# Kernel tuning notes

Hardware: AMD Instinct MI355X
Metric: run time of the kernel (lower is better)

The kernel has to match this reference:

```python
import jax, jax.numpy as jnp
import numpy as np

N, C, H, W = 2, 128, 64, 64
N_HEAD = 4
GROUPS = 16
EPS = 1e-5


def group_norm(x, scale, offset):
    # haiku GroupNorm, channels_first: normalize over (channels-in-group, h, w)
    n, c, h, w = x.shape
    xg = x.reshape(n, GROUPS, c // GROUPS, h, w)
    mu = xg.mean(axis=(2, 3, 4), keepdims=True)
    var = xg.var(axis=(2, 3, 4), keepdims=True)
    xg = (xg - mu) * jax.lax.rsqrt(var + EPS)
    return xg.reshape(n, c, h, w) * scale[None, :, None, None] + offset[None, :, None, None]


def setup_inputs() -> dict:
    key = jax.random.key(0)
    ks = jax.random.split(key, 4)
    inv_sqrt_c = 1.0 / np.sqrt(C).astype(np.float32)
    return {
        "x": jax.random.normal(ks[0], (N, C, H, W), dtype=jnp.float32),
        "w_qkv": jax.random.normal(ks[1], (C, 3 * C), dtype=jnp.float32) * inv_sqrt_c,
        "b_qkv": jnp.zeros((3 * C,), dtype=jnp.float32),
        "w_out": jax.random.normal(ks[2], (C, C), dtype=jnp.float32) * inv_sqrt_c,
        "b_out": jnp.zeros((C,), dtype=jnp.float32),
        "gn1_scale": jnp.ones((C,), dtype=jnp.float32),
        "gn1_offset": jnp.zeros((C,), dtype=jnp.float32),
        "gn2_scale": jnp.ones((C,), dtype=jnp.float32),
        "gn2_offset": jnp.zeros((C,), dtype=jnp.float32),
    }


def reference(x, w_qkv, b_qkv, w_out, b_out, gn1_scale, gn1_offset, gn2_scale, gn2_offset):
    n, c, h, w = x.shape
    dh = c // N_HEAD
    # GroupNorm (x is reassigned, so the residual uses the normalized x)
    xn = group_norm(x, gn1_scale, gn1_offset)
    # 1x1 conv qkv projection: [n, 3c, h, w]
    qkv = jnp.einsum('nchw,cd->ndhw', xn, w_qkv) + b_qkv[None, :, None, None]
    # [n, 3H, dh, hw] -> [n, 3H, hw, dh]
    qkv = jnp.swapaxes(qkv.reshape(n, N_HEAD * 3, dh, h * w), 2, 3)
    q, k, v = jnp.split(qkv, 3, axis=1)  # each [n, H, hw, dh]
    scale = dh ** (-0.25)
    # [n, H, hw, hw] attention matrix (the memory-bound core)
    att = jax.nn.softmax((q * scale) @ (jnp.swapaxes(k, 2, 3) * scale), axis=3)
    y = jnp.swapaxes(att @ v, 2, 3).reshape(n, c, h, w)
    # 1x1 conv out projection + GroupNorm + residual
    out = jnp.einsum('nchw,cd->ndhw', y, w_out) + b_out[None, :, None, None]
    return xn + group_norm(out, gn2_scale, gn2_offset)
```

## Files before the change

### kernel.cpp

```cpp
#include <hip/hip_runtime.h>
#include <hip/hip_bf16.h>
#include <math.h>

constexpr int cHW   = 4096;
constexpr int cC    = 128;
constexpr int cNH   = 4;
constexpr int cDH   = 32;
constexpr float cEPS = 1e-5f;
constexpr float cQS = 0.2550347805f;
constexpr int SPLIT = 4;

typedef short bh8  __attribute__((ext_vector_type(8)));
typedef float f4   __attribute__((ext_vector_type(4)));
typedef float f16a __attribute__((ext_vector_type(16)));

static __device__ __forceinline__ unsigned short f2bf(float f) {
  union { __hip_bfloat16 h; unsigned short u; } cv;
  cv.h = __float2bfloat16(f);
  return cv.u;
}
static __device__ __forceinline__ unsigned pack2bf(float a, float b) {
  return (unsigned)f2bf(a) | ((unsigned)f2bf(b) << 16);
}
static __device__ __forceinline__ unsigned pack_trunc(float a, float b) {
  unsigned ua = __builtin_bit_cast(unsigned, a);
  unsigned ub = __builtin_bit_cast(unsigned, b);
  return (ua >> 16) | (ub & 0xffff0000u);
}
static __device__ __forceinline__ float bflo(unsigned pk) {
  return __builtin_bit_cast(float, pk << 16);
}
static __device__ __forceinline__ float bfhi(unsigned pk) {
  return __builtin_bit_cast(float, pk & 0xffff0000u);
}
static __device__ __forceinline__ void plswap(unsigned& a, unsigned& b) {
#if __has_builtin(__builtin_amdgcn_permlane32_swap)
  typedef int v2i __attribute__((ext_vector_type(2)));
  v2i r = __builtin_amdgcn_permlane32_swap((int)a, (int)b, false, false);
  a = (unsigned)r[0]; b = (unsigned)r[1];
#else
  asm("v_permlane32_swap_b32 %0, %1" : "+v"(a), "+v"(b));
#endif
}
static __device__ __forceinline__ bh8 mk8(unsigned a, unsigned b, unsigned c, unsigned d) {
  union { unsigned u[4]; bh8 v; } t;
  t.u[0] = a; t.u[1] = b; t.u[2] = c; t.u[3] = d;
  return t.v;
}

__device__ __forceinline__ void block_reduce2(float& a, float& b, float* sbuf) {
  #pragma unroll
  for (int off = 32; off > 0; off >>= 1) {
    a += __shfl_down(a, off, 64);
    b += __shfl_down(b, off, 64);
  }
  int wave = threadIdx.x >> 6;
  int lane = threadIdx.x & 63;
  if (lane == 0) { sbuf[wave] = a; sbuf[4 + wave] = b; }
  __syncthreads();
  if (threadIdx.x == 0) {
    sbuf[8] = sbuf[0] + sbuf[1] + sbuf[2] + sbuf[3];
    sbuf[9] = sbuf[4] + sbuf[5] + sbuf[6] + sbuf[7];
  }
  __syncthreads();
  a = sbuf[8];
  b = sbuf[9];
}

__global__ __launch_bounds__(256)
void prep(const float* __restrict__ x, float* __restrict__ part,
          const float* __restrict__ wq, const float* __restrict__ wo,
          unsigned short* __restrict__ wqT, unsigned short* __restrict__ woT) {
  __shared__ float lds[32 * 133];
  int L = threadIdx.x;
  if (blockIdx.x < 256) {
    int ng = blockIdx.x >> 3, sl = blockIdx.x & 7;
    const float4* s4 = (const float4*)x;
    float s = 0.f, s2 = 0.f;
    #pragma unroll
    for (int i = 0; i < 4; i++) {
      int idx = i * 256 + L;
      int c = idx >> 7, tt = idx & 127;
      float4 v = s4[(size_t)(ng * 8 + c) * 1024 + sl * 128 + tt];
      s  += v.x + v.y + v.z + v.w;
      s2 += v.x*v.x + v.y*v.y + v.z*v.z + v.w*v.w;
    }
    block_reduce2(s, s2, lds);
    if (L == 0) { part[blockIdx.x * 2] = s; part[blockIdx.x * 2 + 1] = s2; }
  } else {
    int bx = blockIdx.x - 256;
    const float* src; unsigned short* dst; int W, d0;
    if (bx < 12) { src = wq; dst = wqT; W = 384; d0 = bx * 32; }
    else         { src = wo; dst = woT; W = 128; d0 = (bx - 12) * 32; }
    #pragma unroll
    for (int i = 0; i < 16; i++) {
      int c = i * 8 + (L >> 5), d = L & 31;
      lds[d * 133 + c] = src[(size_t)c * W + d0 + d];
    }
    __syncthreads();
    int d = L >> 3, ch = L & 7, c0 = ch * 16;
    unsigned pk[8];
    #pragma unroll
    for (int j = 0; j < 8; j++)
      pk[j] = pack2bf(lds[d * 133 + c0 + 2 * j], lds[d * 133 + c0 + 2 * j + 1]);
    uint4* d4 = (uint4*)(dst + (size_t)(d0 + d) * 128 + c0);
    d4[0] = make_uint4(pk[0], pk[1], pk[2], pk[3]);
    d4[1] = make_uint4(pk[4], pk[5], pk[6], pk[7]);
  }
}

__global__ __launch_bounds__(256)
void gn_stats(const float* __restrict__ src, float* __restrict__ part) {
  __shared__ float sbuf[10];
  int ng = blockIdx.x >> 3, sl = blockIdx.x & 7;
  const float4* s4 = (const float4*)src;
  float s = 0.f, s2 = 0.f;
  #pragma unroll
  for (int i = 0; i < 4; i++) {
    int idx = i * 256 + threadIdx.x;
    int c = idx >> 7, tt = idx & 127;
    float4 v = s4[(size_t)(ng * 8 + c) * 1024 + sl * 128 + tt];
    s  += v.x + v.y + v.z + v.w;
    s2 += v.x*v.x + v.y*v.y + v.z*v.z + v.w*v.w;
  }
  block_reduce2(s, s2, sbuf);
  if (threadIdx.x == 0) { part[blockIdx.x * 2] = s; part[blockIdx.x * 2 + 1] = s2; }
}

__global__ __launch_bounds__(256)
void gn1_pack(const float* __restrict__ x, const float* __restrict__ part,
              const float* __restrict__ sc, const float* __restrict__ of,
              unsigned short* __restrict__ xnB) {
  int cc = blockIdx.x, ts = blockIdx.y, n = blockIdx.z;
  int ng = n * 16 + cc;
  float s = 0.f, s2 = 0.f;
  #pragma unroll
  for (int p = 0; p < 8; p++) { s += part[(ng*8+p)*2]; s2 += part[(ng*8+p)*2+1]; }
  float mu = s * (1.0f / 32768.0f);
  float rinv = rsqrtf(s2 * (1.0f / 32768.0f) - mu * mu + cEPS);
  int t = ts * 256 + threadIdx.x;
  float v[8];
  #pragma unroll
  for (int j = 0; j < 8; j++) {
    int c = cc * 8 + j;
    float a = rinv * sc[c];
    float bo = of[c] - mu * a;
    v[j] = x[((size_t)n * cC + c) * cHW + t] * a + bo;
  }
  unsigned pk[4];
  #pragma unroll
  for (int j = 0; j < 4; j++) pk[j] = pack2bf(v[2*j], v[2*j+1]);
  ((uint4*)xnB)[(size_t)(n * 16 + cc) * cHW + t] = make_uint4(pk[0], pk[1], pk[2], pk[3]);
}

__global__ __launch_bounds__(256)
void qkv_mfma(const unsigned short* __restrict__ xnB, const unsigned short* __restrict__ wqT,
              const float* __restrict__ bq, unsigned* __restrict__ qB,
              unsigned* __restrict__ kB, unsigned* __restrict__ vI) {
  __shared__ float vbuf[64 * 36];
  const int L = threadIdx.x & 63, w = threadIdx.x >> 6;
  const int c16 = L & 15, q = L >> 4;
  const int t0 = blockIdx.x * 64, dg = blockIdx.y, n = blockIdx.z;
  const int nh = n * 4 + (dg & 3), d0 = dg * 32;
  const f4 zf = {0.f, 0.f, 0.f, 0.f};
  f4 acc0 = zf, acc1 = zf;
  const int trow = t0 + w * 16 + c16;
  #pragma unroll
  for (int ks = 0; ks < 4; ks++) {
    bh8 a  = *(const bh8*)(xnB + ((size_t)(n * 16 + ks * 4 + q) * cHW + trow) * 8);
    bh8 b0 = *(const bh8*)(wqT + (size_t)(d0 + c16) * 128 + ks * 32 + q * 8);
    bh8 b1 = *(const bh8*)(wqT + (size_t)(d0 + 16 + c16) * 128 + ks * 32 + q * 8);
    acc0 = __builtin_amdgcn_mfma_f32_16x16x32_bf16(a, b0, acc0, 0, 0, 0);
    acc1 = __builtin_amdgcn_mfma_f32_16x16x32_bf16(a, b1, acc1, 0, 0, 0);
  }
  float blo = bq[d0 + c16], bhi = bq[d0 + 16 + c16];
  if (dg < 8) {
    float scl = (dg < 4) ? cQS : 1.0f;
    unsigned* dst = (dg < 4) ? qB : kB;
    #pragma unroll
    for (int r = 0; r < 4; r++) {
      unsigned pk = pack2bf((acc0[r] + blo) * scl, (acc1[r] + bhi) * scl);
      dst[((size_t)nh * cHW + t0 + w * 16 + q * 4 + r) * 16 + c16] = pk;
    }
  } else {
    #pragma unroll
    for (int r = 0; r < 4; r++) {
      vbuf[(w * 16 + q * 4 + r) * 36 + c16]      = acc0[r] + blo;
      vbuf[(w * 16 + q * 4 + r) * 36 + 16 + c16] = acc1[r] + bhi;
    }
    __syncthreads();
    int t16 = threadIdx.x & 15, dh8 = (threadIdx.x >> 4) & 15;
    #pragma unroll
    for (int blk = 0; blk < 2; blk++)
      #pragma unroll
      for (int hh = 0; hh < 2; hh++) {
        int dh = dh8 + hh * 16;
        float lo = vbuf[(blk * 32 + 2 * t16) * 36 + dh];
        float hi = vbuf[(blk * 32 + 2 * t16 + 1) * 36 + dh];
        vI[((size_t)nh * 32 + dh) * 2048 + (size_t)(t0 / 32 + blk) * 16 + t16] = pack2bf(lo, hi);
      }
  }
}

__global__ __launch_bounds__(256, 4)
void flash_mfma(const unsigned short* __restrict__ qB,
                const unsigned short* __restrict__ kB,
                const unsigned short* __restrict__ vI,
                unsigned* __restrict__ opart, float* __restrict__ lpart) {
  const int w = threadIdx.x >> 6, L = threadIdx.x & 63;
  const int col = L & 31, hi = L >> 5;
  const int qt = blockIdx.x * 4 + w, nh = blockIdx.y, ph = blockIdx.z;
  const short oneb = 0x3F80;
  const bh8 ones = {oneb, oneb, oneb, oneb, oneb, oneb, oneb, oneb};
  const f16a zf16 = {0.f,0.f,0.f,0.f, 0.f,0.f,0.f,0.f, 0.f,0.f,0.f,0.f, 0.f,0.f,0.f,0.f};

  const unsigned short* qb = qB + ((size_t)nh * cHW + (size_t)qt * 32) * cDH;
  bh8 qf0 = *(const bh8*)(qb + (size_t)col * cDH + hi * 8);
  bh8 qf1 = *(const bh8*)(qb + (size_t)col * cDH + 16 + hi * 8);

  const unsigned short* kb = kB + (size_t)nh * cHW * cDH;
  const unsigned short* vb = vI + (size_t)nh * cDH * cHW + (size_t)col * cHW + hi * 8;

  f16a o = zf16, lacc = zf16;

  const int kbeg = ph * (cHW / SPLIT);
  const int kend = kbeg + cHW / SPLIT;

  for (int kt = kbeg; kt < kend; kt += 64) {
    #pragma unroll
    for (int st = 0; st < 2; st++) {
      const int ktb = kt + st * 32;
      bh8 vfa = *(const bh8*)(vb + ktb);
      bh8 vfb = *(const bh8*)(vb + ktb + 16);
      const unsigned short* krow = kb + (size_t)(ktb + col) * cDH;
      bh8 ka0 = *(const bh8*)(krow + hi * 8);
      bh8 ka1 = *(const bh8*)(krow + 16 + hi * 8);
      f16a s = __builtin_amdgcn_mfma_f32_32x32x16_bf16(ka0, qf0, zf16, 0, 0, 0);
      s = __builtin_amdgcn_mfma_f32_32x32x16_bf16(ka1, qf1, s, 0, 0, 0);
      #pragma unroll
      for (int r = 0; r < 16; r++) s[r] = __builtin_amdgcn_exp2f(s[r]);
      unsigned pk0 = pack_trunc(s[0],  s[1]);
      unsigned pk1 = pack_trunc(s[2],  s[3]);
      unsigned pk2 = pack_trunc(s[4],  s[5]);
      unsigned pk3 = pack_trunc(s[6],  s[7]);
      unsigned pk4 = pack_trunc(s[8],  s[9]);
      unsigned pk5 = pack_trunc(s[10], s[11]);
      unsigned pk6 = pack_trunc(s[12], s[13]);
      unsigned pk7 = pack_trunc(s[14], s[15]);
      plswap(pk0, pk2); plswap(pk1, pk3);
      plswap(pk4, pk6); plswap(pk5, pk7);
      bh8 pf0 = mk8(pk0, pk1, pk2, pk3);
      bh8 pf1 = mk8(pk4, pk5, pk6, pk7);
      o    = __builtin_amdgcn_mfma_f32_32x32x16_bf16(pf0, vfa,  o,    0, 0, 0);
      lacc = __builtin_amdgcn_mfma_f32_32x32x16_bf16(pf0, ones, lacc, 0, 0, 0);
      o    = __builtin_amdgcn_mfma_f32_32x32x16_bf16(pf1, vfb,  o,    0, 0, 0);
      lacc = __builtin_amdgcn_mfma_f32_32x32x16_bf16(pf1, ones, lacc, 0, 0, 0);
    }
  }

  const size_t base = (size_t)ph * 32768 + (size_t)nh * cHW + (size_t)qt * 32;
  #pragma unroll
  for (int k = 0; k < 8; k++) {
    const int rowlo = ((2 * k) & 3) + 8 * (k >> 1) + 4 * hi;
    opart[((base + rowlo) >> 1) * 32 + col] = pack_trunc(o[2 * k], o[2 * k + 1]);
  }
  if (col == 0) {
    #pragma unroll
    for (int r = 0; r < 16; r++)
      lpart[base + (r & 3) + 8 * (r >> 2) + 4 * hi] = lacc[r];
  }
}

__global__ __launch_bounds__(256)
void combine(const unsigned* __restrict__ opart, const float* __restrict__ lpart,
             unsigned* __restrict__ yB) {
  int tid = blockIdx.x * 256 + threadIdx.x;
  size_t rp = (size_t)(tid >> 1);
  int h = tid & 1;
  size_t r0 = rp * 2;
  float l0 = 0.f, l1 = 0.f;
  #pragma unroll
  for (int p = 0; p < SPLIT; p++) {
    l0 += lpart[(size_t)p * 32768 + r0];
    l1 += lpart[(size_t)p * 32768 + r0 + 1];
  }
  float e0[16], e1[16];
  #pragma unroll
  for (int j = 0; j < 16; j++) { e0[j] = 0.f; e1[j] = 0.f; }
  #pragma unroll
  for (int p = 0; p < SPLIT; p++) {
    const uint4* op = (const uint4*)(opart + ((size_t)p * 16384 + rp) * 32 + h * 16);
    #pragma unroll
    for (int j = 0; j < 4; j++) {
      uint4 v = op[j];
      e0[j*4+0] += bflo(v.x); e1[j*4+0] += bfhi(v.x);
      e0[j*4+1] += bflo(v.y); e1[j*4+1] += bfhi(v.y);
      e0[j*4+2] += bflo(v.z); e1[j*4+2] += bfhi(v.z);
      e0[j*4+3] += bflo(v.w); e1[j*4+3] += bfhi(v.w);
    }
  }
  float i0 = 1.0f / l0, i1 = 1.0f / l1;
  unsigned pkA[8], pkB[8];
  #pragma unroll
  for (int j = 0; j < 8; j++) {
    pkA[j] = pack2bf(e0[2*j] * i0, e0[2*j+1] * i0);
    pkB[j] = pack2bf(e1[2*j] * i1, e1[2*j+1] * i1);
  }
  uint4* dA = (uint4*)(yB + r0 * 16 + h * 8);
  dA[0] = make_uint4(pkA[0], pkA[1], pkA[2], pkA[3]);
  dA[1] = make_uint4(pkA[4], pkA[5], pkA[6], pkA[7]);
  uint4* dB = (uint4*)(yB + (r0 + 1) * 16 + h * 8);
  dB[0] = make_uint4(pkB[0], pkB[1], pkB[2], pkB[3]);
  dB[1] = make_uint4(pkB[4], pkB[5], pkB[6], pkB[7]);
}

__global__ __launch_bounds__(256)
void out_mfma(const unsigned short* __restrict__ yB, const unsigned short* __restrict__ woT,
              const float* __restrict__ bo, float* __restrict__ proj) {
  __shared__ float obuf[64 * 36];
  const int L = threadIdx.x & 63, w = threadIdx.x >> 6;
  const int c16 = L & 15, q = L >> 4;
  const int t0 = blockIdx.x * 64, d0 = blockIdx.y * 32, n = blockIdx.z;
  const f4 zf = {0.f, 0.f, 0.f, 0.f};
  f4 acc0 = zf, acc1 = zf;
  const int trow = t0 + w * 16 + c16;
  #pragma unroll
  for (int h = 0; h < 4; h++) {
    bh8 a  = *(const bh8*)(yB + ((size_t)(n * 4 + h) * cHW + trow) * 32 + q * 8);
    bh8 b0 = *(const bh8*)(woT + (size_t)(d0 + c16) * 128 + h * 32 + q * 8);
    bh8 b1 = *(const bh8*)(woT + (size_t)(d0 + 16 + c16) * 128 + h * 32 + q * 8);
    acc0 = __builtin_amdgcn_mfma_f32_16x16x32_bf16(a, b0, acc0, 0, 0, 0);
    acc1 = __builtin_amdgcn_mfma_f32_16x16x32_bf16(a, b1, acc1, 0, 0, 0);
  }
  float blo = bo[d0 + c16], bhi = bo[d0 + 16 + c16];
  #pragma unroll
  for (int r = 0; r < 4; r++) {
    obuf[(w * 16 + q * 4 + r) * 36 + c16]      = acc0[r] + blo;
    obuf[(w * 16 + q * 4 + r) * 36 + 16 + c16] = acc1[r] + bhi;
  }
  __syncthreads();
  int t16 = threadIdx.x & 15, d8 = (threadIdx.x >> 4) & 15;
  #pragma unroll
  for (int tc = 0; tc < 4; tc++)
    #pragma unroll
    for (int hh = 0; hh < 2; hh++) {
      int d = d8 + hh * 16;
      proj[((size_t)n * cC + d0 + d) * cHW + t0 + tc * 16 + t16] =
          obuf[(tc * 16 + t16) * 36 + d];
    }
}

__global__ __launch_bounds__(256)
void gn2_apply(const float* __restrict__ x, const float* __restrict__ proj,
               const float* __restrict__ p1, const float* __restrict__ p2,
               const float* __restrict__ s1, const float* __restrict__ o1,
               const float* __restrict__ s2, const float* __restrict__ o2,
               float* __restrict__ out) {
  int tid = blockIdx.x * 256 + threadIdx.x;
  int Cg = tid >> 8;
  int n = Cg >> 7, ch = Cg & 127, g = ch >> 3, ng = n * 16 + g;
  float sa = 0.f, sb = 0.f, ta = 0.f, tb = 0.f;
  #pragma unroll
  for (int p = 0; p < 8; p++) {
    sa += p1[(ng*8+p)*2]; sb += p1[(ng*8+p)*2+1];
    ta += p2[(ng*8+p)*2]; tb += p2[(ng*8+p)*2+1];
  }
  float mu1 = sa * (1.0f/32768.0f);
  float ri1 = rsqrtf(sb * (1.0f/32768.0f) - mu1*mu1 + cEPS);
  float a1 = ri1 * s1[ch], b1 = o1[ch] - mu1 * a1;
  float mu2 = ta * (1.0f/32768.0f);
  float ri2 = rsqrtf(tb * (1.0f/32768.0f) - mu2*mu2 + cEPS);
  float a2 = ri2 * s2[ch], b2 = o2[ch] - mu2 * a2;
  const float4* x4 = (const float4*)x;
  const float4* pr4 = (const float4*)proj;
  float4* o4 = (float4*)out;
  #pragma unroll
  for (int i = 0; i < 4; i++) {
    size_t f = (size_t)tid * 4 + i;
    float4 xv = x4[f], pv = pr4[f];
    float4 r;
    r.x = xv.x * a1 + b1 + pv.x * a2 + b2;
    r.y = xv.y * a1 + b1 + pv.y * a2 + b2;
    r.z = xv.z * a1 + b1 + pv.z * a2 + b2;
    r.w = xv.w * a1 + b1 + pv.w * a2 + b2;
    o4[f] = r;
  }
}

extern "C" void kernel_launch(void* const* d_in, const int* in_sizes, int n_in,
                              void* d_out, int out_size, void* d_ws, size_t ws_size,
                              hipStream_t stream) {
  const float* x     = (const float*)d_in[0];
  const float* w_qkv = (const float*)d_in[1];
  const float* b_qkv = (const float*)d_in[2];
  const float* w_out = (const float*)d_in[3];
  const float* b_out = (const float*)d_in[4];
  const float* g1s   = (const float*)d_in[5];
  const float* g1o   = (const float*)d_in[6];
  const float* g2s   = (const float*)d_in[7];
  const float* g2o   = (const float*)d_in[8];
  float* out = (float*)d_out;
  float* ws  = (float*)d_ws;

  const size_t MAP = (size_t)2 * cC * cHW;
  float* proj    = ws;
  float* lpart   = proj + MAP;
  float* stats1  = lpart + (size_t)SPLIT * 32768;
  float* stats2  = stats1 + 512;
  unsigned* opart = (unsigned*)(stats2 + 512);
  unsigned* qB   = opart + (size_t)SPLIT * 32768 * 16;
  unsigned* kB   = qB + MAP / 2;
  unsigned* vI   = kB + MAP / 2;
  unsigned* yB   = vI + MAP / 2;
  unsigned short* xnB = (unsigned short*)(yB + MAP / 2);
  unsigned short* wqT = xnB + MAP;
  unsigned short* woT = wqT + 49152;

  prep      <<<dim3(272),           256, 0, stream>>>(x, stats1, w_qkv, w_out, wqT, woT);
  gn1_pack  <<<dim3(16, 16, 2),     256, 0, stream>>>(x, stats1, g1s, g1o, xnB);
  qkv_mfma  <<<dim3(64, 12, 2),     256, 0, stream>>>(xnB, wqT, b_qkv, qB, kB, vI);
  flash_mfma<<<dim3(32, 8, SPLIT),  256, 0, stream>>>((const unsigned short*)qB,
                                                      (const unsigned short*)kB,
                                                      (const unsigned short*)vI,
                                                      opart, lpart);
  combine   <<<dim3(128),           256, 0, stream>>>(opart, lpart, yB);
  out_mfma  <<<dim3(64, 4, 2),      256, 0, stream>>>((const unsigned short*)yB, woT,
                                                      b_out, proj);
  gn_stats  <<<dim3(256),           256, 0, stream>>>(proj, stats2);
  gn2_apply <<<dim3(256),           256, 0, stream>>>(x, proj, stats1, stats2,
                                                      g1s, g1o, g2s, g2o, out);
}
```

Baseline: 148.8 us.

## Store Q/K/V in MFMA fragment-ordered layout for contiguous per-lane loads

The QKV projection kernel now stages all outputs through shared memory and writes Q, K and V pre-arranged in the exact per-lane MFMA operand order, as one 16-byte store per thread. The flash attention loop then reads each 32-key tile with fully contiguous 16-byte loads per lane instead of strided row gathers. This is meant to cut memory transactions and address arithmetic in the attention inner loop. In exchange, every QKV block now pays an LDS round trip and a barrier, and the loop is unrolled by 2.

Result: faster. 130.9 us (-12.0%).

```diff
diff --git a/kernel.cpp b/kernel.cpp
--- a/kernel.cpp
+++ b/kernel.cpp
@@ -155,8 +155,8 @@
 
 __global__ __launch_bounds__(256)
 void qkv_mfma(const unsigned short* __restrict__ xnB, const unsigned short* __restrict__ wqT,
-              const float* __restrict__ bq, unsigned* __restrict__ qB,
-              unsigned* __restrict__ kB, unsigned* __restrict__ vI) {
+              const float* __restrict__ bq, unsigned* __restrict__ qF,
+              unsigned* __restrict__ kF, unsigned* __restrict__ vF) {
   __shared__ float vbuf[64 * 36];
   const int L = threadIdx.x & 63, w = threadIdx.x >> 6;
   const int c16 = L & 15, q = L >> 4;
@@ -173,39 +173,35 @@
     acc0 = __builtin_amdgcn_mfma_f32_16x16x32_bf16(a, b0, acc0, 0, 0, 0);
     acc1 = __builtin_amdgcn_mfma_f32_16x16x32_bf16(a, b1, acc1, 0, 0, 0);
   }
-  float blo = bq[d0 + c16], bhi = bq[d0 + 16 + c16];
+  const float blo = bq[d0 + c16], bhi = bq[d0 + 16 + c16];
+  const float scl = (dg < 4) ? cQS : 1.0f;
+  #pragma unroll
+  for (int r = 0; r < 4; r++) {
+    vbuf[(w * 16 + q * 4 + r) * 36 + c16]      = (acc0[r] + blo) * scl;
+    vbuf[(w * 16 + q * 4 + r) * 36 + 16 + c16] = (acc1[r] + bhi) * scl;
+  }
+  __syncthreads();
+  const int tl = threadIdx.x >> 7, fr = (threadIdx.x >> 6) & 1, LL = threadIdx.x & 63;
+  const int col = LL & 31, h2 = LL >> 5;
+  unsigned pk[4];
   if (dg < 8) {
-    float scl = (dg < 4) ? cQS : 1.0f;
-    unsigned* dst = (dg < 4) ? qB : kB;
-    #pragma unroll
-    for (int r = 0; r < 4; r++) {
-      unsigned pk = pack2bf((acc0[r] + blo) * scl, (acc1[r] + bhi) * scl);
-      dst[((size_t)nh * cHW + t0 + w * 16 + q * 4 + r) * 16 + c16] = pk;
-    }
+    const float* src = &vbuf[(tl * 32 + col) * 36 + fr * 16 + h2 * 8];
+    #pragma unroll
+    for (int jj = 0; jj < 4; jj++) pk[jj] = pack2bf(src[2 * jj], src[2 * jj + 1]);
   } else {
-    #pragma unroll
-    for (int r = 0; r < 4; r++) {
-      vbuf[(w * 16 + q * 4 + r) * 36 + c16]      = acc0[r] + blo;
-      vbuf[(w * 16 + q * 4 + r) * 36 + 16 + c16] = acc1[r] + bhi;
-    }
-    __syncthreads();
-    int t16 = threadIdx.x & 15, dh8 = (threadIdx.x >> 4) & 15;
-    #pragma unroll
-    for (int blk = 0; blk < 2; blk++)
-      #pragma unroll
-      for (int hh = 0; hh < 2; hh++) {
-        int dh = dh8 + hh * 16;
-        float lo = vbuf[(blk * 32 + 2 * t16) * 36 + dh];
-        float hi = vbuf[(blk * 32 + 2 * t16 + 1) * 36 + dh];
-        vI[((size_t)nh * 32 + dh) * 2048 + (size_t)(t0 / 32 + blk) * 16 + t16] = pack2bf(lo, hi);
-      }
-  }
+    const float* src = &vbuf[(tl * 32 + fr * 16 + h2 * 8) * 36 + col];
+    #pragma unroll
+    for (int jj = 0; jj < 4; jj++) pk[jj] = pack2bf(src[2 * jj * 36], src[(2 * jj + 1) * 36]);
+  }
+  unsigned* dst = (dg < 4) ? qF : ((dg < 8) ? kF : vF);
+  size_t frag = ((size_t)(nh * 128 + (t0 >> 5) + tl) * 2 + fr) * 64 + LL;
+  ((uint4*)dst)[frag] = make_uint4(pk[0], pk[1], pk[2], pk[3]);
 }
 
 __global__ __launch_bounds__(256, 4)
-void flash_mfma(const unsigned short* __restrict__ qB,
-                const unsigned short* __restrict__ kB,
-                const unsigned short* __restrict__ vI,
+void flash_mfma(const unsigned short* __restrict__ qF,
+                const unsigned short* __restrict__ kF,
+                const unsigned short* __restrict__ vF,
                 unsigned* __restrict__ opart, float* __restrict__ lpart) {
   const int w = threadIdx.x >> 6, L = threadIdx.x & 63;
   const int col = L & 31, hi = L >> 5;
@@ -214,48 +210,44 @@
   const bh8 ones = {oneb, oneb, oneb, oneb, oneb, oneb, oneb, oneb};
   const f16a zf16 = {0.f,0.f,0.f,0.f, 0.f,0.f,0.f,0.f, 0.f,0.f,0.f,0.f, 0.f,0.f,0.f,0.f};
 
-  const unsigned short* qb = qB + ((size_t)nh * cHW + (size_t)qt * 32) * cDH;
-  bh8 qf0 = *(const bh8*)(qb + (size_t)col * cDH + hi * 8);
-  bh8 qf1 = *(const bh8*)(qb + (size_t)col * cDH + 16 + hi * 8);
-
-  const unsigned short* kb = kB + (size_t)nh * cHW * cDH;
-  const unsigned short* vb = vI + (size_t)nh * cDH * cHW + (size_t)col * cHW + hi * 8;
+  const unsigned short* qb = qF + ((size_t)(nh * 128 + qt) * 2) * 512;
+  bh8 qf0 = *(const bh8*)(qb + L * 8);
+  bh8 qf1 = *(const bh8*)(qb + 512 + L * 8);
+
+  const unsigned short* kb = kF + (size_t)nh * 128 * 1024;
+  const unsigned short* vb = vF + (size_t)nh * 128 * 1024;
 
   f16a o = zf16, lacc = zf16;
 
-  const int kbeg = ph * (cHW / SPLIT);
-  const int kend = kbeg + cHW / SPLIT;
-
-  for (int kt = kbeg; kt < kend; kt += 64) {
-    #pragma unroll
-    for (int st = 0; st < 2; st++) {
-      const int ktb = kt + st * 32;
-      bh8 vfa = *(const bh8*)(vb + ktb);
-      bh8 vfb = *(const bh8*)(vb + ktb + 16);
-      const unsigned short* krow = kb + (size_t)(ktb + col) * cDH;
-      bh8 ka0 = *(const bh8*)(krow + hi * 8);
-      bh8 ka1 = *(const bh8*)(krow + 16 + hi * 8);
-      f16a s = __builtin_amdgcn_mfma_f32_32x32x16_bf16(ka0, qf0, zf16, 0, 0, 0);
-      s = __builtin_amdgcn_mfma_f32_32x32x16_bf16(ka1, qf1, s, 0, 0, 0);
-      #pragma unroll
-      for (int r = 0; r < 16; r++) s[r] = __builtin_amdgcn_exp2f(s[r]);
-      unsigned pk0 = pack_trunc(s[0],  s[1]);
-      unsigned pk1 = pack_trunc(s[2],  s[3]);
-      unsigned pk2 = pack_trunc(s[4],  s[5]);
-      unsigned pk3 = pack_trunc(s[6],  s[7]);
-      unsigned pk4 = pack_trunc(s[8],  s[9]);
-      unsigned pk5 = pack_trunc(s[10], s[11]);
-      unsigned pk6 = pack_trunc(s[12], s[13]);
-      unsigned pk7 = pack_trunc(s[14], s[15]);
-      plswap(pk0, pk2); plswap(pk1, pk3);
-      plswap(pk4, pk6); plswap(pk5, pk7);
-      bh8 pf0 = mk8(pk0, pk1, pk2, pk3);
-      bh8 pf1 = mk8(pk4, pk5, pk6, pk7);
-      o    = __builtin_amdgcn_mfma_f32_32x32x16_bf16(pf0, vfa,  o,    0, 0, 0);
-      lacc = __builtin_amdgcn_mfma_f32_32x32x16_bf16(pf0, ones, lacc, 0, 0, 0);
-      o    = __builtin_amdgcn_mfma_f32_32x32x16_bf16(pf1, vfb,  o,    0, 0, 0);
-      lacc = __builtin_amdgcn_mfma_f32_32x32x16_bf16(pf1, ones, lacc, 0, 0, 0);
-    }
+  const int tb0 = ph * (cHW / SPLIT / 32);
+  #pragma unroll 2
+  for (int tl = tb0; tl < tb0 + 32; ++tl) {
+    const unsigned short* kp = kb + (size_t)tl * 1024;
+    const unsigned short* vp = vb + (size_t)tl * 1024;
+    bh8 ka0 = *(const bh8*)(kp + L * 8);
+    bh8 ka1 = *(const bh8*)(kp + 512 + L * 8);
+    bh8 vfa = *(const bh8*)(vp + L * 8);
+    bh8 vfb = *(const bh8*)(vp + 512 + L * 8);
+    f16a s = __builtin_amdgcn_mfma_f32_32x32x16_bf16(ka0, qf0, zf16, 0, 0, 0);
+    s = __builtin_amdgcn_mfma_f32_32x32x16_bf16(ka1, qf1, s, 0, 0, 0);
+    #pragma unroll
+    for (int r = 0; r < 16; r++) s[r] = __builtin_amdgcn_exp2f(s[r]);
+    unsigned pk0 = pack_trunc(s[0],  s[1]);
+    unsigned pk1 = pack_trunc(s[2],  s[3]);
+    unsigned pk2 = pack_trunc(s[4],  s[5]);
+    unsigned pk3 = pack_trunc(s[6],  s[7]);
+    unsigned pk4 = pack_trunc(s[8],  s[9]);
+    unsigned pk5 = pack_trunc(s[10], s[11]);
+    unsigned pk6 = pack_trunc(s[12], s[13]);
+    unsigned pk7 = pack_trunc(s[14], s[15]);
+    plswap(pk0, pk2); plswap(pk1, pk3);
+    plswap(pk4, pk6); plswap(pk5, pk7);
+    bh8 pf0 = mk8(pk0, pk1, pk2, pk3);
+    bh8 pf1 = mk8(pk4, pk5, pk6, pk7);
+    o    = __builtin_amdgcn_mfma_f32_32x32x16_bf16(pf0, vfa,  o,    0, 0, 0);
+    lacc = __builtin_amdgcn_mfma_f32_32x32x16_bf16(pf0, ones, lacc, 0, 0, 0);
+    o    = __builtin_amdgcn_mfma_f32_32x32x16_bf16(pf1, vfb,  o,    0, 0, 0);
+    lacc = __builtin_amdgcn_mfma_f32_32x32x16_bf16(pf1, ones, lacc, 0, 0, 0);
   }
 
   const size_t base = (size_t)ph * 32768 + (size_t)nh * cHW + (size_t)qt * 32;
@@ -408,20 +400,20 @@
   float* stats1  = lpart + (size_t)SPLIT * 32768;
   float* stats2  = stats1 + 512;
   unsigned* opart = (unsigned*)(stats2 + 512);
-  unsigned* qB   = opart + (size_t)SPLIT * 32768 * 16;
-  unsigned* kB   = qB + MAP / 2;
-  unsigned* vI   = kB + MAP / 2;
-  unsigned* yB   = vI + MAP / 2;
+  unsigned* qF   = opart + (size_t)SPLIT * 32768 * 16;
+  unsigned* kF   = qF + MAP / 2;
+  unsigned* vF   = kF + MAP / 2;
+  unsigned* yB   = vF + MAP / 2;
   unsigned short* xnB = (unsigned short*)(yB + MAP / 2);
   unsigned short* wqT = xnB + MAP;
   unsigned short* woT = wqT + 49152;
 
   prep      <<<dim3(272),           256, 0, stream>>>(x, stats1, w_qkv, w_out, wqT, woT);
   gn1_pack  <<<dim3(16, 16, 2),     256, 0, stream>>>(x, stats1, g1s, g1o, xnB);
-  qkv_mfma  <<<dim3(64, 12, 2),     256, 0, stream>>>(xnB, wqT, b_qkv, qB, kB, vI);
-  flash_mfma<<<dim3(32, 8, SPLIT),  256, 0, stream>>>((const unsigned short*)qB,
-                                                      (const unsigned short*)kB,
-                                                      (const unsigned short*)vI,
+  qkv_mfma  <<<dim3(64, 12, 2),     256, 0, stream>>>(xnB, wqT, b_qkv, qF, kF, vF);
+  flash_mfma<<<dim3(32, 8, SPLIT),  256, 0, stream>>>((const unsigned short*)qF,
+                                                      (const unsigned short*)kF,
+                                                      (const unsigned short*)vF,
                                                       opart, lpart);
   combine   <<<dim3(128),           256, 0, stream>>>(opart, lpart, yB);
   out_mfma  <<<dim3(64, 4, 2),      256, 0, stream>>>((const unsigned short*)yB, woT,
```
